# Optimization experiments

Hardware: AMD Instinct MI355X
Metric: run time of the kernel (lower is better)

Reference implementation:

```python
import jax, jax.numpy as jnp
import numpy as np
from jax import lax

B, U, L, H, V, NSPK, R, E = 8, 32, 64, 512, 32000, 16, 4, 128
S = U * L

def setup_inputs() -> dict:
    key = jax.random.key(0)
    ks = jax.random.split(key, 14)
    sc = lambda k, shape, fan: (jax.random.normal(k, shape, jnp.float32) / np.sqrt(fan)).astype(jnp.float32)
    src = jax.random.randint(ks[0], (S, B, 1), 0, V)
    speaker = jax.random.randint(ks[1], (B, S), 0, NSPK)
    seg = jnp.tile(jnp.arange(U + 1) * L, (B, 1))  # uniform utterance boundaries
    lengths = jnp.full((B,), S, dtype=jnp.int32)
    edge_src = jax.random.randint(ks[2], (B, E), 0, U + 1)
    edge_dst = jax.random.randint(ks[3], (B, E), 0, U + 1)
    rels = jax.random.randint(ks[4], (B, E), 0, R)
    return {
        'src': src, 'seg': seg, 'speaker': speaker, 'lengths': lengths,
        'edge_src': edge_src, 'edge_dst': edge_dst, 'rels': rels,
        'emb_table': sc(ks[5], (V, H), H), 'spk_table': sc(ks[6], (NSPK, H), H),
        'W_ih': sc(ks[7], (H, 4 * H), H), 'W_hh': sc(ks[8], (H, 4 * H), H),
        'b_lstm': jnp.zeros((4 * H,), jnp.float32),
        'W_rel': sc(ks[9], (R, H, H), H), 'W_self': sc(ks[10], (H, H), H),
        'b_gnn': jnp.zeros((H,), jnp.float32),
        'Wg1': sc(ks[11], (H, H), H), 'Wg2': sc(ks[12], (H, H), H),
    }

def _forward(src, seg, speaker, lengths, edge_src, edge_dst, rels,
             emb_table, spk_table, W_ih, W_hh, b_lstm, W_rel, W_self, b_gnn, Wg1, Wg2):
    # src: [S, B, 1] -> words [B, S]; uniform segmentation -> utterances [B*U, L]
    words = src[:, :, 0].T
    utts = words.reshape(B * U, L)
    spk = speaker.reshape(B * U, L)
    x = emb_table[utts] + spk_table[spk]            # [N, L, H]
    xs = x.transpose(1, 0, 2)                        # [L, N, H]
    N = B * U
    h0 = jnp.zeros((N, H), x.dtype)

    def step(carry, xt):
        h, c = carry
        gates = xt @ W_ih + h @ W_hh + b_lstm
        i, f, g, o = jnp.split(gates, 4, axis=-1)
        c = jax.nn.sigmoid(f) * c + jax.nn.sigmoid(i) * jnp.tanh(g)
        h = jax.nn.sigmoid(o) * jnp.tanh(c)
        return (h, c), h

    (hT, cT), ys = lax.scan(step, (h0, h0), xs)      # ys: [L, N, H]
    # word-level memory bank scattered back to meeting layout -> [S, B, H]
    memory_bank = ys.transpose(1, 0, 2).reshape(B, S, H).transpose(1, 0, 2)

    # graph over U utterance nodes + 1 global node per meeting
    utt_h = hT.reshape(B, U, H)
    gnode = utt_h.mean(axis=1, keepdims=True)
    nodes = jnp.concatenate([utt_h, gnode], axis=1)  # [B, U+1, H]
    x_src = jnp.take_along_axis(nodes, edge_src[..., None], axis=1)  # [B, E, H]
    msg = jnp.zeros_like(x_src)
    for r in range(R):
        msg = msg + jnp.where((rels == r)[..., None], x_src @ W_rel[r], 0.0)
    agg = jax.vmap(lambda m, d: jax.ops.segment_sum(m, d, num_segments=U + 1))(msg, edge_dst)
    out = jax.nn.relu(nodes @ W_self + agg + b_gnn)
    gate = jax.nn.sigmoid(nodes @ Wg1 + agg @ Wg2)
    new_nodes = gate * out + (1.0 - gate) * nodes
    global_reps = new_nodes[:, -1]                   # [B, H]
    utt_upd = new_nodes[:, :U]                       # [B, U, H]

    # utterance-level memory bank: repeat each utterance rep over its words
    mbu = jnp.broadcast_to(utt_upd[:, :, None, :], (B, U, L, H)).reshape(B, S, H).transpose(1, 0, 2)
    hier_matrix = jnp.full((B, S), jnp.float32(L))
    enc_h = global_reps[None]                        # [1, B, H]
    enc_c = enc_h
    return (enc_h, enc_c), memory_bank, lengths, mbu, lengths, hier_matrix

def reference(src, seg, speaker, lengths, edge_src, edge_dst, rels,
              emb_table, spk_table, W_ih, W_hh, b_lstm, W_rel, W_self, b_gnn, Wg1, Wg2):
    return _forward(src, seg, speaker, lengths, edge_src, edge_dst, rels,
                    emb_table, spk_table, W_ih, W_hh, b_lstm, W_rel, W_self, b_gnn, Wg1, Wg2)
```

## Files before the change

kernel.cpp:

```cpp
#include <hip/hip_runtime.h>
#include <hip/hip_bf16.h>
#include <math.h>

typedef __bf16 bf16x8 __attribute__((ext_vector_type(8)));
typedef float  f32x4  __attribute__((ext_vector_type(4)));


#define OFF_ENCH 0
#define OFF_ENCC 4096
#define OFF_MB   8192
#define OFF_LEN1 8396800
#define OFF_MBU  8396808
#define OFF_LEN2 16785416
#define OFF_HIER 16785424

#define WS_X     0
#define WS_WIH   16777216
#define WS_WHH   18874368
#define WS_HBUF  20971520
#define WS_CBUF  21495808
#define WS_NODES 22020096
#define WS_AGG   22560768
#define WS_NEWN  23101440
#define WS_XG    23642112
#define WS_SPLIT_NEED 90750976ull
#define ZERO_WORDS 532480

__device__ __forceinline__ float sigm(float x) { return 1.0f / (1.0f + expf(-x)); }

__device__ __forceinline__ void async_cp16(const __bf16* g, __bf16* l) {
    __builtin_amdgcn_global_load_lds((const __attribute__((address_space(1))) void*)g,
                                     (__attribute__((address_space(3))) void*)l,
                                     16, 0, 0);
}

__global__ __launch_bounds__(256) void k_init(unsigned int* zero_base,
                                              const int* lengths, float* out)
{
    int idx = blockIdx.x * 256 + threadIdx.x;
    if (idx < ZERO_WORDS) { zero_base[idx] = 0u; return; }
    int j = idx - ZERO_WORDS;
    if (j < 16384) { out[OFF_HIER + j] = 64.0f; return; }
    int j2 = j - 16384;
    if (j2 < 16) {
        float v = (float)lengths[j2 & 7];
        out[(j2 < 8 ? OFF_LEN1 : OFF_LEN2) + (j2 & 7)] = v;
    }
}

__global__ __launch_bounds__(256) void k_cvtw(const float* __restrict__ Wih,
                                              const float* __restrict__ Whh,
                                              __bf16* __restrict__ WihT,
                                              __bf16* __restrict__ WhhT)
{
    __shared__ float tile[64][65];
    int gid = blockIdx.x;
    const float* Wsrc = (gid >> 8) ? Whh : Wih;
    __bf16*      Wdst = (gid >> 8) ? WhhT : WihT;
    int rem = gid & 255;
    int k0 = (rem >> 5) << 6;
    int c0 = (rem & 31) << 6;
    int tid = threadIdx.x;
#pragma unroll
    for (int i = 0; i < 16; ++i) {
        int idx = tid + i * 256;
        int kl = idx >> 6, cl = idx & 63;
        tile[cl][kl] = Wsrc[(size_t)(k0 + kl) * 2048 + c0 + cl];
    }
    __syncthreads();
#pragma unroll
    for (int i = 0; i < 16; ++i) {
        int idx = tid + i * 256;
        int cl = idx >> 6, kl = idx & 63;
        Wdst[(size_t)(c0 + cl) * 512 + k0 + kl] = (__bf16)tile[cl][kl];
    }
}

__global__ __launch_bounds__(256) void k_embed(const int* __restrict__ src,
                                               const int* __restrict__ speaker,
                                               const float* __restrict__ emb,
                                               const float* __restrict__ spk,
                                               __bf16* __restrict__ X)
{
    int tid = blockIdx.x * 256 + threadIdx.x;
    int p  = tid >> 6;
    int k8 = (tid & 63) << 3;
    int t = p >> 8, n = p & 255;
    int b = n >> 5, u = n & 31;
    int s = u * 64 + t;
    int word = src[s * 8 + b];
    int sid  = speaker[b * 2048 + s];
    f32x4 e0 = *(const f32x4*)&emb[word * 512 + k8];
    f32x4 e1 = *(const f32x4*)&emb[word * 512 + k8 + 4];
    f32x4 s0 = *(const f32x4*)&spk[sid * 512 + k8];
    f32x4 s1 = *(const f32x4*)&spk[sid * 512 + k8 + 4];
    bf16x8 o;
#pragma unroll
    for (int j = 0; j < 4; ++j) {
        o[j]     = (__bf16)(e0[j] + s0[j]);
        o[4 + j] = (__bf16)(e1[j] + s1[j]);
    }
    *(bf16x8*)&X[p * 512 + k8] = o;
}

__global__ __launch_bounds__(256) void k_gemm_xg(const __bf16* __restrict__ X,
                                                 const __bf16* __restrict__ Wt,
                                                 const float* __restrict__ bl,
                                                 __bf16* __restrict__ Xg)
{
    __shared__ __bf16 As[128 * 32];
    __shared__ __bf16 Bs[128 * 32];
    int tid = threadIdx.x;
    int w = tid >> 6, lane = tid & 63;
    int ml = lane & 15, q = lane >> 4;
    int m0 = blockIdx.y << 7, n0 = blockIdx.x << 7;
    f32x4 acc[4][4] = {};
    int mb = (w & 1) * 64, nb = (w >> 1) * 64;
    int lr = lane >> 2, lc = (lane & 3) << 3;
    for (int k0 = 0; k0 < 512; k0 += 32) {
#pragma unroll
        for (int i = 0; i < 2; ++i) {
            int r = w * 32 + i * 16;
            async_cp16(X  + (size_t)(m0 + r + lr) * 512 + k0 + lc, &As[r * 32]);
            async_cp16(Wt + (size_t)(n0 + r + lr) * 512 + k0 + lc, &Bs[r * 32]);
        }
        __syncthreads();
        bf16x8 af[4], bf_[4];
#pragma unroll
        for (int mi = 0; mi < 4; ++mi)
            af[mi] = *(const bf16x8*)&As[(mb + mi * 16 + ml) * 32 + q * 8];
#pragma unroll
        for (int ni = 0; ni < 4; ++ni)
            bf_[ni] = *(const bf16x8*)&Bs[(nb + ni * 16 + ml) * 32 + q * 8];
#pragma unroll
        for (int mi = 0; mi < 4; ++mi)
#pragma unroll
            for (int ni = 0; ni < 4; ++ni)
                acc[mi][ni] = __builtin_amdgcn_mfma_f32_16x16x32_bf16(af[mi], bf_[ni], acc[mi][ni], 0, 0, 0);
        __syncthreads();
    }
#pragma unroll
    for (int ni = 0; ni < 4; ++ni) {
        int col = n0 + nb + ni * 16 + ml;
        float bias = bl[col];
#pragma unroll
        for (int mi = 0; mi < 4; ++mi) {
#pragma unroll
            for (int r = 0; r < 4; ++r) {
                int row = m0 + mb + mi * 16 + q * 4 + r;
                Xg[(size_t)row * 2048 + col] = (__bf16)(acc[mi][ni][r] + bias);
            }
        }
    }
}

__global__ __launch_bounds__(256) void k_lstm_step(const __bf16* __restrict__ hin,
                                                   __bf16* __restrict__ hout,
                                                   float* __restrict__ cbuf,
                                                   const __bf16* __restrict__ Xt,
                                                   const __bf16* __restrict__ WihT,
                                                   const __bf16* __restrict__ Xg_t,
                                                   const __bf16* __restrict__ WhhT,
                                                   const float* __restrict__ bl,
                                                   float* __restrict__ out,
                                                   int t, int fused)
{
    __shared__ float red[2][64][17];
    int tid = threadIdx.x;
    int w = tid >> 6, lane = tid & 63;
    int ml = lane & 15, q = lane >> 4;
    int rh = w & 1, kh = w >> 1;
    int n0 = blockIdx.y << 5;
    int j0 = blockIdx.x << 4;
    f32x4 acc[4] = {};
    const __bf16* Arow = hin + (size_t)(n0 + rh * 16 + ml) * 512 + kh * 256 + q * 8;
    const __bf16* B0   = WhhT + (size_t)(j0 + ml) * 512 + kh * 256 + q * 8;
#pragma unroll
    for (int k0 = 0; k0 < 256; k0 += 32) {
        bf16x8 a = *(const bf16x8*)(Arow + k0);
#pragma unroll
        for (int g = 0; g < 4; ++g) {
            bf16x8 b = *(const bf16x8*)(B0 + ((size_t)g << 18) + k0);
            acc[g] = __builtin_amdgcn_mfma_f32_16x16x32_bf16(a, b, acc[g], 0, 0, 0);
        }
    }
    if (fused) {
        const __bf16* A2 = Xt + (size_t)(n0 + rh * 16 + ml) * 512 + kh * 256 + q * 8;
        const __bf16* B2 = WihT + (size_t)(j0 + ml) * 512 + kh * 256 + q * 8;
#pragma unroll
        for (int k0 = 0; k0 < 256; k0 += 32) {
            bf16x8 a = *(const bf16x8*)(A2 + k0);
#pragma unroll
            for (int g = 0; g < 4; ++g) {
                bf16x8 b = *(const bf16x8*)(B2 + ((size_t)g << 18) + k0);
                acc[g] = __builtin_amdgcn_mfma_f32_16x16x32_bf16(a, b, acc[g], 0, 0, 0);
            }
        }
    }
    if (kh == 1) {
#pragma unroll
        for (int g = 0; g < 4; ++g)
#pragma unroll
            for (int r = 0; r < 4; ++r)
                red[rh][lane][g * 4 + r] = acc[g][r];
    }
    __syncthreads();
    if (kh == 1) return;
#pragma unroll
    for (int g = 0; g < 4; ++g)
#pragma unroll
        for (int r = 0; r < 4; ++r)
            acc[g][r] += red[rh][lane][g * 4 + r];

    int jc = j0 + ml;
#pragma unroll
    for (int r = 0; r < 4; ++r) {
        int n = n0 + rh * 16 + q * 4 + r;
        int b = n >> 5, u = n & 31;
        int s = u * 64 + t;
        float pi, pf, pg, po;
        if (fused) {
            pi = acc[0][r] + bl[jc];
            pf = acc[1][r] + bl[512 + jc];
            pg = acc[2][r] + bl[1024 + jc];
            po = acc[3][r] + bl[1536 + jc];
        } else {
            const __bf16* xg = Xg_t + (size_t)n * 2048;
            pi = acc[0][r] + (float)xg[jc];
            pf = acc[1][r] + (float)xg[512 + jc];
            pg = acc[2][r] + (float)xg[1024 + jc];
            po = acc[3][r] + (float)xg[1536 + jc];
        }
        float ig = sigm(pi), fg = sigm(pf);
        float gg = tanhf(pg), og = sigm(po);
        float cn = fg * cbuf[n * 512 + jc] + ig * gg;
        cbuf[n * 512 + jc] = cn;
        float hn = og * tanhf(cn);
        hout[n * 512 + jc] = (__bf16)hn;
        out[OFF_MB + ((size_t)s * 8 + b) * 512 + jc] = hn;
    }
}

__global__ __launch_bounds__(256) void k_nodes(const __bf16* __restrict__ hT,
                                               float* __restrict__ nodes)
{
    int b = blockIdx.x;
    for (int k = threadIdx.x; k < 512; k += 256) {
        float sum = 0.f;
        for (int u = 0; u < 32; ++u) {
            float v = (float)hT[(b * 32 + u) * 512 + k];
            nodes[(b * 33 + u) * 512 + k] = v;
            sum += v;
        }
        nodes[(b * 33 + 32) * 512 + k] = sum * (1.0f / 32.0f);
    }
}

__global__ __launch_bounds__(256) void k_edges(const float* __restrict__ nodes,
                                               const int* __restrict__ edge_src,
                                               const int* __restrict__ edge_dst,
                                               const int* __restrict__ rels,
                                               const float* __restrict__ Wrel,
                                               float* __restrict__ agg)
{
    __shared__ float xs[512];
    int eg = blockIdx.x;
    int b = eg >> 7, e = eg & 127;
    int es = edge_src[b * 128 + e];
    int ed = edge_dst[b * 128 + e];
    int r  = rels[b * 128 + e];
    int tid = threadIdx.x;
    for (int k = tid; k < 512; k += 256) xs[k] = nodes[(b * 33 + es) * 512 + k];
    __syncthreads();
    const float* Wr = Wrel + r * 262144;
    float a0 = 0.f, a1 = 0.f;
#pragma unroll 4
    for (int k = 0; k < 512; ++k) {
        float xk = xs[k];
        a0 += xk * Wr[k * 512 + tid];
        a1 += xk * Wr[k * 512 + 256 + tid];
    }
    atomicAdd(&agg[(b * 33 + ed) * 512 + tid], a0);
    atomicAdd(&agg[(b * 33 + ed) * 512 + 256 + tid], a1);
}

__global__ __launch_bounds__(256) void k_gnn(const float* __restrict__ nodes,
                                             const float* __restrict__ agg,
                                             const float* __restrict__ Wself,
                                             const float* __restrict__ bgnn,
                                             const float* __restrict__ Wg1,
                                             const float* __restrict__ Wg2,
                                             float* __restrict__ newn,
                                             float* __restrict__ out)
{
    __shared__ float nd[512], ag[512];
    __shared__ float red[4][3][64];
    int vg = blockIdx.x;
    int j0 = blockIdx.y << 6;
    int b = vg / 33, v = vg % 33;
    int tid = threadIdx.x;
    for (int k = tid; k < 512; k += 256) {
        nd[k] = nodes[vg * 512 + k];
        ag[k] = agg[vg * 512 + k];
    }
    __syncthreads();
    int jl = tid & 63, kq = tid >> 6;
    int jj = j0 + jl;
    int kbase = kq << 7;
    float a_s = 0.f, a1 = 0.f, a2 = 0.f;
#pragma unroll 4
    for (int kk = 0; kk < 128; ++kk) {
        int k = kbase + kk;
        float ndk = nd[k], agk = ag[k];
        a_s += ndk * Wself[k * 512 + jj];
        a1  += ndk * Wg1[k * 512 + jj];
        a2  += agk * Wg2[k * 512 + jj];
    }
    red[kq][0][jl] = a_s;
    red[kq][1][jl] = a1;
    red[kq][2][jl] = a2;
    __syncthreads();
    if (tid < 64) {
        int j = j0 + tid;
        float s0 = red[0][0][tid] + red[1][0][tid] + red[2][0][tid] + red[3][0][tid];
        float s1 = red[0][1][tid] + red[1][1][tid] + red[2][1][tid] + red[3][1][tid];
        float s2 = red[0][2][tid] + red[1][2][tid] + red[2][2][tid] + red[3][2][tid];
        float outv = fmaxf(s0 + ag[j] + bgnn[j], 0.f);
        float gate = sigm(s1 + s2);
        float newv = gate * outv + (1.f - gate) * nd[j];
        newn[vg * 512 + j] = newv;
        if (v == 32) {
            out[OFF_ENCH + b * 512 + j] = newv;
            out[OFF_ENCC + b * 512 + j] = newv;
        }
    }
}

__global__ __launch_bounds__(256) void k_mbu(const float* __restrict__ newn,
                                             float* __restrict__ out)
{
    int idx = blockIdx.x * 256 + threadIdx.x;
    int k8 = (idx & 63) << 3;
    int rest = idx >> 6;
    int b = rest & 7;
    int s = rest >> 3;
    int u = s >> 6;
    const float* sp = &newn[(b * 33 + u) * 512 + k8];
    f32x4 v0 = *(const f32x4*)sp;
    f32x4 v1 = *(const f32x4*)(sp + 4);
    float* dp = &out[OFF_MBU + (s * 8 + b) * 512 + k8];
    *(f32x4*)dp = v0;
    *(f32x4*)(dp + 4) = v1;
}

extern "C" void kernel_launch(void* const* d_in, const int* in_sizes, int n_in,
                              void* d_out, int out_size, void* d_ws, size_t ws_size,
                              hipStream_t stream)
{
    (void)in_sizes; (void)n_in; (void)out_size;
    const int*   src      = (const int*)d_in[0];
    const int*   speaker  = (const int*)d_in[2];
    const int*   lengths  = (const int*)d_in[3];
    const int*   edge_src = (const int*)d_in[4];
    const int*   edge_dst = (const int*)d_in[5];
    const int*   rels     = (const int*)d_in[6];
    const float* emb   = (const float*)d_in[7];
    const float* spk   = (const float*)d_in[8];
    const float* Wih   = (const float*)d_in[9];
    const float* Whh   = (const float*)d_in[10];
    const float* bl    = (const float*)d_in[11];
    const float* Wrel  = (const float*)d_in[12];
    const float* Wself = (const float*)d_in[13];
    const float* bgnn  = (const float*)d_in[14];
    const float* Wg1   = (const float*)d_in[15];
    const float* Wg2   = (const float*)d_in[16];
    float* out = (float*)d_out;
    char*  ws  = (char*)d_ws;

    __bf16* X     = (__bf16*)(ws + WS_X);
    __bf16* WihT  = (__bf16*)(ws + WS_WIH);
    __bf16* WhhT  = (__bf16*)(ws + WS_WHH);
    __bf16* hb0   = (__bf16*)(ws + WS_HBUF);
    __bf16* hb1   = hb0 + 131072;
    float*  cbuf  = (float*)(ws + WS_CBUF);
    float*  nodes = (float*)(ws + WS_NODES);
    float*  agg   = (float*)(ws + WS_AGG);
    float*  newn  = (float*)(ws + WS_NEWN);
    __bf16* Xg    = (__bf16*)(ws + WS_XG);

    int split = (ws_size >= WS_SPLIT_NEED) ? 1 : 0;

    k_init<<<2145, 256, 0, stream>>>((unsigned int*)(ws + WS_HBUF), lengths, out);
    k_cvtw<<<512, 256, 0, stream>>>(Wih, Whh, WihT, WhhT);
    k_embed<<<4096, 256, 0, stream>>>(src, speaker, emb, spk, X);
    if (split)
        k_gemm_xg<<<dim3(16, 128), 256, 0, stream>>>(X, WihT, bl, Xg);
    for (int t = 0; t < 64; ++t) {
        const __bf16* hin = (t & 1) ? hb1 : hb0;
        __bf16* hout      = (t & 1) ? hb0 : hb1;
        k_lstm_step<<<dim3(32, 8), 256, 0, stream>>>(
            hin, hout, cbuf,
            X + (size_t)t * 131072, WihT,
            Xg + (size_t)t * 524288, WhhT, bl,
            out, t, split ? 0 : 1);
    }
    k_nodes<<<8, 256, 0, stream>>>(hb0, nodes);
    k_edges<<<1024, 256, 0, stream>>>(nodes, edge_src, edge_dst, rels, Wrel, agg);
    k_gnn<<<dim3(264, 8), 256, 0, stream>>>(nodes, agg, Wself, bgnn, Wg1, Wg2, newn, out);
    k_mbu<<<4096, 256, 0, stream>>>(newn, out);
}
```

Measured before the change: 980.4 us.

## Fuse LSTM time loop into persistent kernel with grid barrier; MFMA edge GEMM

Replaces the 64 per-timestep LSTM launches and the separate input-projection GEMM with one persistent kernel of 256 blocks. Each block keeps its slice of W_hh and W_ih in registers, holds the cell state in registers, and syncs the grid through an atomic counter/epoch barrier between timesteps. The per-edge scalar GNN relation matmul becomes a bf16 MFMA GEMM over all relations with masked atomic scatter, using a newly pre-transposed bf16 W_rel. The persistent kernel depends on all 256 blocks being resident at once, and the large register arrays risk spilling. The edge GEMM computes every relation for every edge and keeps only the matching one, so it does redundant work.

```diff
diff --git a/kernel.cpp b/kernel.cpp
--- a/kernel.cpp
+++ b/kernel.cpp
@@ -14,17 +14,17 @@
 #define OFF_LEN2 16785416
 #define OFF_HIER 16785424
 
-#define WS_X     0
-#define WS_WIH   16777216
-#define WS_WHH   18874368
-#define WS_HBUF  20971520
-#define WS_CBUF  21495808
-#define WS_NODES 22020096
-#define WS_AGG   22560768
-#define WS_NEWN  23101440
-#define WS_XG    23642112
-#define WS_SPLIT_NEED 90750976ull
-#define ZERO_WORDS 532480
+#define WS_X      0
+#define WS_WIH    16777216
+#define WS_WHH    18874368
+#define WS_HBUF   20971520
+#define WS_BAR    21495808
+#define WS_AGG    21499904
+#define WS_NODES  22040576
+#define WS_NODESB 22581248
+#define WS_NEWN   22851584
+#define WS_WRELT  23392256
+#define ZERO_WORDS 267264
 
 __device__ __forceinline__ float sigm(float x) { return 1.0f / (1.0f + expf(-x)); }
 
@@ -50,29 +50,53 @@
 
 __global__ __launch_bounds__(256) void k_cvtw(const float* __restrict__ Wih,
                                               const float* __restrict__ Whh,
+                                              const float* __restrict__ Wrel,
                                               __bf16* __restrict__ WihT,
-                                              __bf16* __restrict__ WhhT)
+                                              __bf16* __restrict__ WhhT,
+                                              __bf16* __restrict__ WrelT)
 {
     __shared__ float tile[64][65];
     int gid = blockIdx.x;
-    const float* Wsrc = (gid >> 8) ? Whh : Wih;
-    __bf16*      Wdst = (gid >> 8) ? WhhT : WihT;
-    int rem = gid & 255;
-    int k0 = (rem >> 5) << 6;
-    int c0 = (rem & 31) << 6;
     int tid = threadIdx.x;
-#pragma unroll
-    for (int i = 0; i < 16; ++i) {
-        int idx = tid + i * 256;
-        int kl = idx >> 6, cl = idx & 63;
-        tile[cl][kl] = Wsrc[(size_t)(k0 + kl) * 2048 + c0 + cl];
-    }
-    __syncthreads();
-#pragma unroll
-    for (int i = 0; i < 16; ++i) {
-        int idx = tid + i * 256;
-        int cl = idx >> 6, kl = idx & 63;
-        Wdst[(size_t)(c0 + cl) * 512 + k0 + kl] = (__bf16)tile[cl][kl];
+    if (gid < 512) {
+        const float* Wsrc = (gid >> 8) ? Whh : Wih;
+        __bf16*      Wdst = (gid >> 8) ? WhhT : WihT;
+        int rem = gid & 255;
+        int k0 = (rem >> 5) << 6;
+        int c0 = (rem & 31) << 6;
+#pragma unroll
+        for (int i = 0; i < 16; ++i) {
+            int idx = tid + i * 256;
+            int kl = idx >> 6, cl = idx & 63;
+            tile[cl][kl] = Wsrc[(size_t)(k0 + kl) * 2048 + c0 + cl];
+        }
+        __syncthreads();
+#pragma unroll
+        for (int i = 0; i < 16; ++i) {
+            int idx = tid + i * 256;
+            int cl = idx >> 6, kl = idx & 63;
+            Wdst[(size_t)(c0 + cl) * 512 + k0 + kl] = (__bf16)tile[cl][kl];
+        }
+    } else {
+        int rem = gid - 512;
+        int r = rem >> 6;
+        int t6 = rem & 63;
+        int k0 = (t6 >> 3) << 6, j0 = (t6 & 7) << 6;
+        const float* src = Wrel + (size_t)r * 262144;
+        __bf16*      dst = WrelT + (size_t)r * 262144;
+#pragma unroll
+        for (int i = 0; i < 16; ++i) {
+            int idx = tid + i * 256;
+            int kl = idx >> 6, jl = idx & 63;
+            tile[jl][kl] = src[(size_t)(k0 + kl) * 512 + j0 + jl];
+        }
+        __syncthreads();
+#pragma unroll
+        for (int i = 0; i < 16; ++i) {
+            int idx = tid + i * 256;
+            int jl = idx >> 6, kl = idx & 63;
+            dst[(size_t)(j0 + jl) * 512 + k0 + kl] = (__bf16)tile[jl][kl];
+        }
     }
 }
 
@@ -103,146 +127,113 @@
     *(bf16x8*)&X[p * 512 + k8] = o;
 }
 
-__global__ __launch_bounds__(256) void k_gemm_xg(const __bf16* __restrict__ X,
-                                                 const __bf16* __restrict__ Wt,
-                                                 const float* __restrict__ bl,
-                                                 __bf16* __restrict__ Xg)
-{
-    __shared__ __bf16 As[128 * 32];
-    __shared__ __bf16 Bs[128 * 32];
-    int tid = threadIdx.x;
-    int w = tid >> 6, lane = tid & 63;
-    int ml = lane & 15, q = lane >> 4;
-    int m0 = blockIdx.y << 7, n0 = blockIdx.x << 7;
-    f32x4 acc[4][4] = {};
-    int mb = (w & 1) * 64, nb = (w >> 1) * 64;
-    int lr = lane >> 2, lc = (lane & 3) << 3;
-    for (int k0 = 0; k0 < 512; k0 += 32) {
-#pragma unroll
-        for (int i = 0; i < 2; ++i) {
-            int r = w * 32 + i * 16;
-            async_cp16(X  + (size_t)(m0 + r + lr) * 512 + k0 + lc, &As[r * 32]);
-            async_cp16(Wt + (size_t)(n0 + r + lr) * 512 + k0 + lc, &Bs[r * 32]);
-        }
-        __syncthreads();
-        bf16x8 af[4], bf_[4];
-#pragma unroll
-        for (int mi = 0; mi < 4; ++mi)
-            af[mi] = *(const bf16x8*)&As[(mb + mi * 16 + ml) * 32 + q * 8];
-#pragma unroll
-        for (int ni = 0; ni < 4; ++ni)
-            bf_[ni] = *(const bf16x8*)&Bs[(nb + ni * 16 + ml) * 32 + q * 8];
-#pragma unroll
-        for (int mi = 0; mi < 4; ++mi)
-#pragma unroll
-            for (int ni = 0; ni < 4; ++ni)
-                acc[mi][ni] = __builtin_amdgcn_mfma_f32_16x16x32_bf16(af[mi], bf_[ni], acc[mi][ni], 0, 0, 0);
-        __syncthreads();
-    }
-#pragma unroll
-    for (int ni = 0; ni < 4; ++ni) {
-        int col = n0 + nb + ni * 16 + ml;
-        float bias = bl[col];
-#pragma unroll
-        for (int mi = 0; mi < 4; ++mi) {
-#pragma unroll
-            for (int r = 0; r < 4; ++r) {
-                int row = m0 + mb + mi * 16 + q * 4 + r;
-                Xg[(size_t)row * 2048 + col] = (__bf16)(acc[mi][ni][r] + bias);
-            }
-        }
-    }
-}
-
-__global__ __launch_bounds__(256) void k_lstm_step(const __bf16* __restrict__ hin,
-                                                   __bf16* __restrict__ hout,
-                                                   float* __restrict__ cbuf,
-                                                   const __bf16* __restrict__ Xt,
-                                                   const __bf16* __restrict__ WihT,
-                                                   const __bf16* __restrict__ Xg_t,
-                                                   const __bf16* __restrict__ WhhT,
-                                                   const float* __restrict__ bl,
-                                                   float* __restrict__ out,
-                                                   int t, int fused)
+__global__ __launch_bounds__(256, 1) void k_lstm_all(const __bf16* __restrict__ X,
+                                                     const __bf16* __restrict__ WihT,
+                                                     const __bf16* __restrict__ WhhT,
+                                                     const float* __restrict__ bl,
+                                                     __bf16* __restrict__ hb0,
+                                                     __bf16* __restrict__ hb1,
+                                                     float* __restrict__ out,
+                                                     int* __restrict__ bar)
 {
     __shared__ float red[2][64][17];
     int tid = threadIdx.x;
     int w = tid >> 6, lane = tid & 63;
     int ml = lane & 15, q = lane >> 4;
     int rh = w & 1, kh = w >> 1;
-    int n0 = blockIdx.y << 5;
-    int j0 = blockIdx.x << 4;
-    f32x4 acc[4] = {};
-    const __bf16* Arow = hin + (size_t)(n0 + rh * 16 + ml) * 512 + kh * 256 + q * 8;
-    const __bf16* B0   = WhhT + (size_t)(j0 + ml) * 512 + kh * 256 + q * 8;
-#pragma unroll
-    for (int k0 = 0; k0 < 256; k0 += 32) {
-        bf16x8 a = *(const bf16x8*)(Arow + k0);
-#pragma unroll
-        for (int g = 0; g < 4; ++g) {
-            bf16x8 b = *(const bf16x8*)(B0 + ((size_t)g << 18) + k0);
-            acc[g] = __builtin_amdgcn_mfma_f32_16x16x32_bf16(a, b, acc[g], 0, 0, 0);
-        }
-    }
-    if (fused) {
-        const __bf16* A2 = Xt + (size_t)(n0 + rh * 16 + ml) * 512 + kh * 256 + q * 8;
-        const __bf16* B2 = WihT + (size_t)(j0 + ml) * 512 + kh * 256 + q * 8;
-#pragma unroll
-        for (int k0 = 0; k0 < 256; k0 += 32) {
-            bf16x8 a = *(const bf16x8*)(A2 + k0);
+    int bx = blockIdx.x;
+    int j0 = (bx & 31) << 4;
+    int n0 = (bx >> 5) << 5;
+    int jc = j0 + ml;
+    int rowA = n0 + rh * 16 + ml;
+    int koff = kh * 256 + q * 8;
+
+    bf16x8 Bh[32], Bi[32];
+    {
+        const __bf16* bh = WhhT + (size_t)jc * 512 + koff;
+        const __bf16* bi = WihT + (size_t)jc * 512 + koff;
+#pragma unroll
+        for (int ki = 0; ki < 8; ++ki)
 #pragma unroll
             for (int g = 0; g < 4; ++g) {
-                bf16x8 b = *(const bf16x8*)(B2 + ((size_t)g << 18) + k0);
-                acc[g] = __builtin_amdgcn_mfma_f32_16x16x32_bf16(a, b, acc[g], 0, 0, 0);
+                Bh[ki * 4 + g] = *(const bf16x8*)(bh + ((size_t)g << 18) + ki * 32);
+                Bi[ki * 4 + g] = *(const bf16x8*)(bi + ((size_t)g << 18) + ki * 32);
             }
-        }
-    }
-    if (kh == 1) {
-#pragma unroll
-        for (int g = 0; g < 4; ++g)
-#pragma unroll
-            for (int r = 0; r < 4; ++r)
-                red[rh][lane][g * 4 + r] = acc[g][r];
-    }
-    __syncthreads();
-    if (kh == 1) return;
-#pragma unroll
-    for (int g = 0; g < 4; ++g)
-#pragma unroll
-        for (int r = 0; r < 4; ++r)
-            acc[g][r] += red[rh][lane][g * 4 + r];
-
-    int jc = j0 + ml;
-#pragma unroll
-    for (int r = 0; r < 4; ++r) {
-        int n = n0 + rh * 16 + q * 4 + r;
-        int b = n >> 5, u = n & 31;
-        int s = u * 64 + t;
-        float pi, pf, pg, po;
-        if (fused) {
-            pi = acc[0][r] + bl[jc];
-            pf = acc[1][r] + bl[512 + jc];
-            pg = acc[2][r] + bl[1024 + jc];
-            po = acc[3][r] + bl[1536 + jc];
-        } else {
-            const __bf16* xg = Xg_t + (size_t)n * 2048;
-            pi = acc[0][r] + (float)xg[jc];
-            pf = acc[1][r] + (float)xg[512 + jc];
-            pg = acc[2][r] + (float)xg[1024 + jc];
-            po = acc[3][r] + (float)xg[1536 + jc];
-        }
-        float ig = sigm(pi), fg = sigm(pf);
-        float gg = tanhf(pg), og = sigm(po);
-        float cn = fg * cbuf[n * 512 + jc] + ig * gg;
-        cbuf[n * 512 + jc] = cn;
-        float hn = og * tanhf(cn);
-        hout[n * 512 + jc] = (__bf16)hn;
-        out[OFF_MB + ((size_t)s * 8 + b) * 512 + jc] = hn;
+    }
+    float bias[4];
+#pragma unroll
+    for (int g = 0; g < 4; ++g) bias[g] = bl[g * 512 + jc];
+    float c[4] = {0.f, 0.f, 0.f, 0.f};
+
+    int* cnt   = bar;
+    int* epoch = bar + 64;
+
+    for (int t = 0; t < 64; ++t) {
+        const __bf16* hrow = (t & 1 ? hb1 : hb0) + (size_t)rowA * 512 + koff;
+        const __bf16* xrow = X + (((size_t)(t << 8) + rowA) << 9) + koff;
+        bf16x8 av[8], xv[8];
+#pragma unroll
+        for (int ki = 0; ki < 8; ++ki) {
+            av[ki] = *(const bf16x8*)(hrow + ki * 32);
+            xv[ki] = *(const bf16x8*)(xrow + ki * 32);
+        }
+        f32x4 acc[4] = {};
+#pragma unroll
+        for (int ki = 0; ki < 8; ++ki)
+#pragma unroll
+            for (int g = 0; g < 4; ++g) {
+                acc[g] = __builtin_amdgcn_mfma_f32_16x16x32_bf16(av[ki], Bh[ki * 4 + g], acc[g], 0, 0, 0);
+                acc[g] = __builtin_amdgcn_mfma_f32_16x16x32_bf16(xv[ki], Bi[ki * 4 + g], acc[g], 0, 0, 0);
+            }
+        if (kh == 1) {
+#pragma unroll
+            for (int g = 0; g < 4; ++g)
+#pragma unroll
+                for (int r = 0; r < 4; ++r)
+                    red[rh][lane][g * 4 + r] = acc[g][r];
+        }
+        __syncthreads();
+        if (kh == 0) {
+            __bf16* hw = (t & 1) ? hb0 : hb1;
+#pragma unroll
+            for (int r = 0; r < 4; ++r) {
+                int n = n0 + rh * 16 + q * 4 + r;
+                float pi = acc[0][r] + red[rh][lane][0 * 4 + r] + bias[0];
+                float pf = acc[1][r] + red[rh][lane][1 * 4 + r] + bias[1];
+                float pg = acc[2][r] + red[rh][lane][2 * 4 + r] + bias[2];
+                float po = acc[3][r] + red[rh][lane][3 * 4 + r] + bias[3];
+                float ig = sigm(pi), fg = sigm(pf);
+                float gg = tanhf(pg), og = sigm(po);
+                float cn = fg * c[r] + ig * gg;
+                c[r] = cn;
+                float hn = og * tanhf(cn);
+                hw[(size_t)n * 512 + jc] = (__bf16)hn;
+                int b = n >> 5, u = n & 31;
+                int s = u * 64 + t;
+                out[OFF_MB + ((size_t)s * 8 + b) * 512 + jc] = hn;
+            }
+        }
+        if (t < 63) {
+            __threadfence();
+            __syncthreads();
+            if (tid == 0) {
+                int prev = __hip_atomic_fetch_add(cnt, 1, __ATOMIC_ACQ_REL, __HIP_MEMORY_SCOPE_AGENT);
+                if (prev == 256 * (t + 1) - 1) {
+                    __hip_atomic_store(epoch, t + 1, __ATOMIC_RELEASE, __HIP_MEMORY_SCOPE_AGENT);
+                } else {
+                    while (__hip_atomic_load(epoch, __ATOMIC_ACQUIRE, __HIP_MEMORY_SCOPE_AGENT) < t + 1)
+                        __builtin_amdgcn_s_sleep(8);
+                }
+            }
+            __syncthreads();
+            __threadfence();
+        }
     }
 }
 
 __global__ __launch_bounds__(256) void k_nodes(const __bf16* __restrict__ hT,
-                                               float* __restrict__ nodes)
+                                               float* __restrict__ nodes,
+                                               __bf16* __restrict__ nodesB)
 {
     int b = blockIdx.x;
     for (int k = threadIdx.x; k < 512; k += 256) {
@@ -250,38 +241,78 @@
         for (int u = 0; u < 32; ++u) {
             float v = (float)hT[(b * 32 + u) * 512 + k];
             nodes[(b * 33 + u) * 512 + k] = v;
+            nodesB[(b * 33 + u) * 512 + k] = (__bf16)v;
             sum += v;
         }
-        nodes[(b * 33 + 32) * 512 + k] = sum * (1.0f / 32.0f);
-    }
-}
-
-__global__ __launch_bounds__(256) void k_edges(const float* __restrict__ nodes,
-                                               const int* __restrict__ edge_src,
-                                               const int* __restrict__ edge_dst,
-                                               const int* __restrict__ rels,
-                                               const float* __restrict__ Wrel,
-                                               float* __restrict__ agg)
-{
-    __shared__ float xs[512];
-    int eg = blockIdx.x;
-    int b = eg >> 7, e = eg & 127;
-    int es = edge_src[b * 128 + e];
-    int ed = edge_dst[b * 128 + e];
-    int r  = rels[b * 128 + e];
+        float gm = sum * (1.0f / 32.0f);
+        nodes[(b * 33 + 32) * 512 + k] = gm;
+        nodesB[(b * 33 + 32) * 512 + k] = (__bf16)gm;
+    }
+}
+
+__global__ __launch_bounds__(256) void k_edges_mm(const __bf16* __restrict__ nodesB,
+                                                  const __bf16* __restrict__ WrelT,
+                                                  const int* __restrict__ edge_src,
+                                                  const int* __restrict__ edge_dst,
+                                                  const int* __restrict__ rels,
+                                                  float* __restrict__ agg)
+{
+    __shared__ __bf16 As[128 * 32];
+    __shared__ __bf16 Bs[128 * 32];
     int tid = threadIdx.x;
-    for (int k = tid; k < 512; k += 256) xs[k] = nodes[(b * 33 + es) * 512 + k];
-    __syncthreads();
-    const float* Wr = Wrel + r * 262144;
-    float a0 = 0.f, a1 = 0.f;
-#pragma unroll 4
-    for (int k = 0; k < 512; ++k) {
-        float xk = xs[k];
-        a0 += xk * Wr[k * 512 + tid];
-        a1 += xk * Wr[k * 512 + 256 + tid];
-    }
-    atomicAdd(&agg[(b * 33 + ed) * 512 + tid], a0);
-    atomicAdd(&agg[(b * 33 + ed) * 512 + 256 + tid], a1);
+    int w = tid >> 6, lane = tid & 63;
+    int ml = lane & 15, q = lane >> 4;
+    int by = blockIdx.y;
+    int n0 = blockIdx.x << 7;
+    int rel = n0 >> 9, jbase = n0 & 511;
+    int mb = (w & 1) * 64, nb = (w >> 1) * 64;
+    int lr = lane >> 2, lc = (lane & 3) << 3;
+    const __bf16* ap[2]; const __bf16* bp[2];
+#pragma unroll
+    for (int i = 0; i < 2; ++i) {
+        int r = w * 32 + i * 16 + lr;
+        int es = edge_src[by * 128 + r];
+        ap[i] = nodesB + ((size_t)by * 33 + es) * 512 + lc;
+        bp[i] = WrelT + (size_t)rel * 262144 + (size_t)(jbase + r) * 512 + lc;
+    }
+    f32x4 acc[4][4] = {};
+    for (int k0 = 0; k0 < 512; k0 += 32) {
+#pragma unroll
+        for (int i = 0; i < 2; ++i) {
+            int r = w * 32 + i * 16;
+            async_cp16(ap[i] + k0, &As[r * 32]);
+            async_cp16(bp[i] + k0, &Bs[r * 32]);
+        }
+        __syncthreads();
+        bf16x8 af[4], bf_[4];
+#pragma unroll
+        for (int mi = 0; mi < 4; ++mi)
+            af[mi] = *(const bf16x8*)&As[(mb + mi * 16 + ml) * 32 + q * 8];
+#pragma unroll
+        for (int ni = 0; ni < 4; ++ni)
+            bf_[ni] = *(const bf16x8*)&Bs[(nb + ni * 16 + ml) * 32 + q * 8];
+#pragma unroll
+        for (int mi = 0; mi < 4; ++mi)
+#pragma unroll
+            for (int ni = 0; ni < 4; ++ni)
+                acc[mi][ni] = __builtin_amdgcn_mfma_f32_16x16x32_bf16(af[mi], bf_[ni], acc[mi][ni], 0, 0, 0);
+        __syncthreads();
+    }
+#pragma unroll
+    for (int mi = 0; mi < 4; ++mi) {
+#pragma unroll
+        for (int r = 0; r < 4; ++r) {
+            int m = mb + mi * 16 + q * 4 + r;
+            int eidx = by * 128 + m;
+            int er = rels[eidx];
+            if (er != rel) continue;
+            int ed = edge_dst[eidx];
+            float* dst = &agg[((size_t)by * 33 + ed) * 512 + jbase];
+#pragma unroll
+            for (int ni = 0; ni < 4; ++ni)
+                atomicAdd(dst + nb + ni * 16 + ml, acc[mi][ni][r]);
+        }
+    }
 }
 
 __global__ __launch_bounds__(256) void k_gnn(const float* __restrict__ nodes,
@@ -357,7 +388,7 @@
                               void* d_out, int out_size, void* d_ws, size_t ws_size,
                               hipStream_t stream)
 {
-    (void)in_sizes; (void)n_in; (void)out_size;
+    (void)in_sizes; (void)n_in; (void)out_size; (void)ws_size;
     const int*   src      = (const int*)d_in[0];
     const int*   speaker  = (const int*)d_in[2];
     const int*   lengths  = (const int*)d_in[3];
@@ -377,35 +408,24 @@
     float* out = (float*)d_out;
     char*  ws  = (char*)d_ws;
 
-    __bf16* X     = (__bf16*)(ws + WS_X);
-    __bf16* WihT  = (__bf16*)(ws + WS_WIH);
-    __bf16* WhhT  = (__bf16*)(ws + WS_WHH);
-    __bf16* hb0   = (__bf16*)(ws + WS_HBUF);
-    __bf16* hb1   = hb0 + 131072;
-    float*  cbuf  = (float*)(ws + WS_CBUF);
-    float*  nodes = (float*)(ws + WS_NODES);
-    float*  agg   = (float*)(ws + WS_AGG);
-    float*  newn  = (float*)(ws + WS_NEWN);
-    __bf16* Xg    = (__bf16*)(ws + WS_XG);
-
-    int split = (ws_size >= WS_SPLIT_NEED) ? 1 : 0;
-
-    k_init<<<2145, 256, 0, stream>>>((unsigned int*)(ws + WS_HBUF), lengths, out);
-    k_cvtw<<<512, 256, 0, stream>>>(Wih, Whh, WihT, WhhT);
+    __bf16* X      = (__bf16*)(ws + WS_X);
+    __bf16* WihT   = (__bf16*)(ws + WS_WIH);
+    __bf16* WhhT   = (__bf16*)(ws + WS_WHH);
+    __bf16* hb0    = (__bf16*)(ws + WS_HBUF);
+    __bf16* hb1    = hb0 + 131072;
+    int*    bar    = (int*)(ws + WS_BAR);
+    float*  agg    = (float*)(ws + WS_AGG);
+    float*  nodes  = (float*)(ws + WS_NODES);
+    __bf16* nodesB = (__bf16*)(ws + WS_NODESB);
+    float*  newn   = (float*)(ws + WS_NEWN);
+    __bf16* WrelT  = (__bf16*)(ws + WS_WRELT);
+
+    k_init<<<1109, 256, 0, stream>>>((unsigned int*)(ws + WS_HBUF), lengths, out);
+    k_cvtw<<<768, 256, 0, stream>>>(Wih, Whh, Wrel, WihT, WhhT, WrelT);
     k_embed<<<4096, 256, 0, stream>>>(src, speaker, emb, spk, X);
-    if (split)
-        k_gemm_xg<<<dim3(16, 128), 256, 0, stream>>>(X, WihT, bl, Xg);
-    for (int t = 0; t < 64; ++t) {
-        const __bf16* hin = (t & 1) ? hb1 : hb0;
-        __bf16* hout      = (t & 1) ? hb0 : hb1;
-        k_lstm_step<<<dim3(32, 8), 256, 0, stream>>>(
-            hin, hout, cbuf,
-            X + (size_t)t * 131072, WihT,
-            Xg + (size_t)t * 524288, WhhT, bl,
-            out, t, split ? 0 : 1);
-    }
-    k_nodes<<<8, 256, 0, stream>>>(hb0, nodes);
-    k_edges<<<1024, 256, 0, stream>>>(nodes, edge_src, edge_dst, rels, Wrel, agg);
+    k_lstm_all<<<256, 256, 0, stream>>>(X, WihT, WhhT, bl, hb0, hb1, out, bar);
+    k_nodes<<<8, 256, 0, stream>>>(hb0, nodes, nodesB);
+    k_edges_mm<<<dim3(16, 8), 256, 0, stream>>>(nodesB, WrelT, edge_src, edge_dst, rels, agg);
     k_gnn<<<dim3(264, 8), 256, 0, stream>>>(nodes, agg, Wself, bgnn, Wg1, Wg2, newn, out);
     k_mbu<<<4096, 256, 0, stream>>>(newn, out);
 }
```

Measured after the change: 3.450 ms. 252% more time.
